# Kernel optimization log

Measured on AMD Instinct MI355X. Metric: run time of the kernel, lower is better.

Reference implementation:

```python
import jax, jax.numpy as jnp
import numpy as np
import math

# Single graph (batch vector identically 0): per-graph topk and global_max_pool
# reduce to static lax.top_k and jnp.max. Pooled edge_index from SAGPooling is
# discarded because KnnEdges rebuilds the graph every layer (no_op=False).
N = 20000      # nodes
HID = 128      # in_channels == hidden_channels
L = 3          # num_layers
RATIO = 0.5    # pool_ratio
K0, KINC = 6, 2  # KnnEdges start_k / k_increment
OUT = 5


def setup_inputs() -> dict:
    key = jax.random.key(0)
    ks = jax.random.split(key, 10)
    s = 0.05  # keep tanh scores unsaturated
    x = jax.random.normal(ks[0], (N, HID), jnp.float32)
    pos = jax.random.uniform(ks[1], (N, 2), jnp.float32) * 100.0
    src = jax.random.randint(ks[2], (N * K0,), 0, N)
    dst = jnp.repeat(jnp.arange(N), K0)
    edge_index = jnp.stack([src, dst]).astype(jnp.int32)  # [2, E], row0=src(j), row1=dst(i)
    return dict(
        x=x, pos=pos, edge_index=edge_index,
        Wrel=jax.random.normal(ks[3], (L, HID, HID), jnp.float32) * s,
        brel=jnp.zeros((L, HID), jnp.float32),
        Wroot=jax.random.normal(ks[4], (L, HID, HID), jnp.float32) * s,
        Wprel=jax.random.normal(ks[5], (L, HID), jnp.float32) * s,
        bprel=jnp.zeros((L,), jnp.float32),
        Wproot=jax.random.normal(ks[6], (L, HID), jnp.float32) * s,
        W1=jax.random.normal(ks[7], (HID * L, HID), jnp.float32) * s,
        b1=jnp.zeros((HID,), jnp.float32),
        W2=jax.random.normal(ks[8], (HID, OUT), jnp.float32) * s,
        b2=jnp.zeros((OUT,), jnp.float32),
    )


def _mean_agg(x, src, dst, n):
    # mean over incoming messages x_j for each target i (PyG aggr='mean'; 0 if isolated)
    ssum = jax.ops.segment_sum(x[src], dst, num_segments=n)
    deg = jax.ops.segment_sum(jnp.ones(src.shape, x.dtype), dst, num_segments=n)
    return ssum / jnp.maximum(deg, 1.0)[:, None]


def reference(x, pos, edge_index, Wrel, brel, Wroot, Wprel, bprel, Wproot, W1, b1, W2, b2):
    src, dst = edge_index[0], edge_index[1]
    n = x.shape[0]
    xs = []
    for i in range(L):
        # GraphConv(aggr='mean'): out_i = W_rel @ mean_j x_j + W_root @ x_i + b
        agg = _mean_agg(x, src, dst, n)
        x = jax.nn.relu(agg @ Wrel[i] + x @ Wroot[i] + brel[i])
        # SAGPooling: score GNN = GraphConv(hid->1, aggr='add'); tanh nonlinearity
        sagg = jax.ops.segment_sum(x[src], dst, num_segments=n)
        score = jnp.tanh(sagg @ Wprel[i] + x @ Wproot[i] + bprel[i])  # [n]
        k_keep = math.ceil(RATIO * n)
        vals, perm = jax.lax.top_k(score, k_keep)
        x = x[perm] * vals[:, None]
        xs.append(jnp.max(x, axis=0))  # global_max_pool (single graph)
        # KnnEdges: pos = pos[perm]; rebuild KNN graph with k = start_k + i*k_increment
        pos = pos[perm]
        n = k_keep
        k = K0 + KINC * i
        d2 = jnp.sum((pos[:, None, :] - pos[None, :, :]) ** 2, axis=-1)  # [n, n]
        d2 = jnp.where(jnp.eye(n, dtype=bool), jnp.inf, d2)  # loop=False
        _, nbr = jax.lax.top_k(-d2, k)  # [n, k] nearest neighbors
        src = nbr.reshape(-1)                 # neighbor j (source)
        dst = jnp.repeat(jnp.arange(n), k)    # query i (target)
    h = jnp.concatenate(xs)  # JumpingKnowledge mode='cat' -> [HID*L]
    h = jax.nn.relu(h @ W1 + b1)  # dropout p=0.5 in eval mode: identity
    return (h @ W2 + b2)[None, :]  # [1, OUT]
```

## Files before the change

### kernel.cpp

```cpp
#include <hip/hip_runtime.h>
#include <hip/hip_bf16.h>
#include <math.h>

#define HID 128
#define PR 20
#define CRPB 32
#define CAND_CAP 8192
#define MAXEQ 8192
#define MAXCELLS 4096

__device__ inline int wave_iscan(int v, int lane) {
#pragma unroll
  for (int off = 1; off < 64; off <<= 1) {
    int o = __shfl_up(v, off, 64);
    if (lane >= off) v += o;
  }
  return v;
}

template <int K>
__global__ __launch_bounds__(256) void k_conv_fused(
    const float* __restrict__ x, const int* __restrict__ src, int n, float invk,
    const float* __restrict__ Wrel, const float* __restrict__ Wroot,
    const float* __restrict__ brel,
    const float* __restrict__ wprel, const float* __restrict__ wproot,
    float* __restrict__ out, float* __restrict__ uo, float* __restrict__ vo) {
  __shared__ float4 sagg4[CRPB][HID / 4];
  __shared__ float4 sx4[CRPB][HID / 4];
  __shared__ int ssrc[CRPB * K];
  int t = threadIdx.x;
  int i0 = blockIdx.x * CRPB;
  const int nK = n * K;
  for (int s = t; s < CRPB * K; s += 256) {
    int gi = i0 * K + s;
    int v = (gi < nK) ? src[gi] : 0;
    ssrc[s] = ((unsigned)v < (unsigned)n) ? v : 0;
  }
  __syncthreads();
  {
    int fq = t & 31, h = t >> 5;
    const float4* x4 = (const float4*)x;
    for (int r = h; r < CRPB; r += 8) {
      int row = i0 + r;
      float4 s = make_float4(0.f, 0.f, 0.f, 0.f);
      float4 xv = make_float4(0.f, 0.f, 0.f, 0.f);
      if (row < n) {
#pragma unroll
        for (int j = 0; j < K; ++j) {
          float4 xx = x4[(size_t)ssrc[r * K + j] * 32 + fq];
          s.x += xx.x; s.y += xx.y; s.z += xx.z; s.w += xx.w;
        }
        xv = x4[(size_t)row * 32 + fq];
      }
      s.x *= invk; s.y *= invk; s.z *= invk; s.w *= invk;
      sagg4[r][fq] = s;
      sx4[r][fq] = xv;
    }
  }
  __syncthreads();
  int q = t & 31, rg = t >> 5;
  const float4* Wrel4  = (const float4*)Wrel;
  const float4* Wroot4 = (const float4*)Wroot;
  float4 bq = ((const float4*)brel)[q];
  float4 acc[4];
#pragma unroll
  for (int rr = 0; rr < 4; ++rr) acc[rr] = bq;
  int rbase = rg * 4;
#pragma unroll 2
  for (int cq = 0; cq < HID / 4; ++cq) {
    float4 w1[4], w2[4];
#pragma unroll
    for (int uu = 0; uu < 4; ++uu) {
      w1[uu] = Wrel4[(cq * 4 + uu) * 32 + q];
      w2[uu] = Wroot4[(cq * 4 + uu) * 32 + q];
    }
#pragma unroll
    for (int rr = 0; rr < 4; ++rr) {
      float4 a  = sagg4[rbase + rr][cq];
      float4 xx = sx4[rbase + rr][cq];
      acc[rr].x += a.x*w1[0].x + a.y*w1[1].x + a.z*w1[2].x + a.w*w1[3].x
                 + xx.x*w2[0].x + xx.y*w2[1].x + xx.z*w2[2].x + xx.w*w2[3].x;
      acc[rr].y += a.x*w1[0].y + a.y*w1[1].y + a.z*w1[2].y + a.w*w1[3].y
                 + xx.x*w2[0].y + xx.y*w2[1].y + xx.z*w2[2].y + xx.w*w2[3].y;
      acc[rr].z += a.x*w1[0].z + a.y*w1[1].z + a.z*w1[2].z + a.w*w1[3].z
                 + xx.x*w2[0].z + xx.y*w2[1].z + xx.z*w2[2].z + xx.w*w2[3].z;
      acc[rr].w += a.x*w1[0].w + a.y*w1[1].w + a.z*w1[2].w + a.w*w1[3].w
                 + xx.x*w2[0].w + xx.y*w2[1].w + xx.z*w2[2].w + xx.w*w2[3].w;
    }
  }
  float4 wplq = ((const float4*)wprel)[q];
  float4 wprq = ((const float4*)wproot)[q];
#pragma unroll
  for (int rr = 0; rr < 4; ++rr) {
    int row = i0 + rbase + rr;
    float4 v = acc[rr];
    v.x = v.x > 0.f ? v.x : 0.f;
    v.y = v.y > 0.f ? v.y : 0.f;
    v.z = v.z > 0.f ? v.z : 0.f;
    v.w = v.w > 0.f ? v.w : 0.f;
    float pu = 0.f, pv = 0.f;
    if (row < n) {
      ((float4*)out)[(size_t)row * 32 + q] = v;
      pu = v.x * wplq.x + v.y * wplq.y + v.z * wplq.z + v.w * wplq.w;
      pv = v.x * wprq.x + v.y * wprq.y + v.z * wprq.z + v.w * wprq.w;
    }
#pragma unroll
    for (int o = 16; o; o >>= 1) {
      pu += __shfl_down(pu, o, 32);
      pv += __shfl_down(pv, o, 32);
    }
    if (q == 0 && row < n) { uo[row] = pu; vo[row] = pv; }
  }
}

template <int K>
__global__ void k_score_lite(const float* __restrict__ u, const float* __restrict__ v,
                             const int* __restrict__ src, const float* __restrict__ bprel,
                             int n, float* __restrict__ score, unsigned* __restrict__ key) {
  int i = blockIdx.x * blockDim.x + threadIdx.x;
  if (i >= n) return;
  float s = v[i] + bprel[0];
#pragma unroll
  for (int j = 0; j < K; ++j) s += u[src[i * K + j]];
  float sc = tanhf(s);
  score[i] = sc;
  unsigned bb = __float_as_uint(sc);
  key[i] = (bb & 0x80000000u) ? ~bb : (bb | 0x80000000u);
}

__global__ __launch_bounds__(128) void k_hist(const unsigned* __restrict__ key, int n4,
                                              unsigned* __restrict__ ghist) {
  __shared__ unsigned lh[1024];
  int t = threadIdx.x;
#pragma unroll
  for (int u = 0; u < 8; ++u) lh[t + u * 128] = 0u;
  __syncthreads();
  int i = blockIdx.x * 128 + t;
  if (i < n4) {
    uint4 kv = ((const uint4*)key)[i];
    atomicAdd(&lh[kv.x >> 22], 1u);
    atomicAdd(&lh[kv.y >> 22], 1u);
    atomicAdd(&lh[kv.z >> 22], 1u);
    atomicAdd(&lh[kv.w >> 22], 1u);
  }
  __syncthreads();
#pragma unroll
  for (int u = 0; u < 8; ++u) {
    unsigned v = lh[t + u * 128];
    if (v) atomicAdd(&ghist[t + u * 128], v);
  }
}

__global__ __launch_bounds__(1024) void k_pick(const unsigned* __restrict__ key, int n, int kk,
                                               const unsigned* __restrict__ ghist,
                                               unsigned* __restrict__ outTG) {
  __shared__ unsigned cand[CAND_CAP];
  __shared__ unsigned hist256[256];
  __shared__ unsigned sh_B, sh_above, sh_cnt, sh_remain, sh_prefix;
  __shared__ int wtA[16], wtB[4];
  int t = threadIdx.x;
  int lane = t & 63, wid = t >> 6;
  unsigned long long lmask = (1ull << lane) - 1ull;
  if (t == 0) sh_cnt = 0u;
  {
    unsigned hv = ghist[t];
    int iv = wave_iscan((int)hv, lane);
    if (lane == 63) wtA[wid] = iv;
    __syncthreads();
    int b = 0, tot = 0;
#pragma unroll
    for (int w2 = 0; w2 < 16; ++w2) { int s = wtA[w2]; if (w2 < wid) b += s; tot += s; }
    unsigned val = (unsigned)(iv + b);
    unsigned above_strict = (unsigned)tot - val;
    unsigned above_incl = above_strict + hv;
    if (above_incl >= (unsigned)kk && above_strict < (unsigned)kk) {
      sh_B = (unsigned)t;
      sh_above = above_strict;
    }
    __syncthreads();
  }
  unsigned B = sh_B, above = sh_above;
  int remain = kk - (int)above;
  for (int i = t; i < n; i += 1024) {
    unsigned kv = key[i];
    bool m = ((kv >> 22) == B);
    unsigned long long mm = __ballot(m);
    if (mm) {
      int leader = (int)(__ffsll((long long)mm) - 1);
      unsigned base = 0;
      if (lane == leader) base = atomicAdd(&sh_cnt, (unsigned)__popcll(mm));
      base = (unsigned)__shfl((int)base, leader, 64);
      if (m) {
        unsigned p = base + (unsigned)__popcll(mm & lmask);
        if (p < CAND_CAP) cand[p] = kv;
      }
    }
  }
  __syncthreads();
  int cnt = (int)sh_cnt; if (cnt > CAND_CAP) cnt = CAND_CAP;
  if (t == 0) { sh_prefix = 0u; sh_remain = (unsigned)remain; }
  __syncthreads();
  for (int pass = 0; pass < 4; ++pass) {
    int shift = 24 - pass * 8;
    unsigned prefix = sh_prefix;
    unsigned rem = sh_remain;
    if (t < 256) hist256[t] = 0u;
    __syncthreads();
    unsigned himask = (pass == 0) ? 0u : (0xFFFFFFFFu << (shift + 8));
    for (int i = t; i < cnt; i += 1024) {
      unsigned kky = cand[i];
      if ((kky & himask) == prefix) atomicAdd(&hist256[(kky >> shift) & 255u], 1u);
    }
    __syncthreads();
    int hv = (t < 256) ? (int)hist256[t] : 0;
    int iv = wave_iscan(hv, lane);
    if (t < 256 && lane == 63) wtB[wid] = iv;
    __syncthreads();
    if (t < 256) {
      int b = 0, tot = 0;
#pragma unroll
      for (int w2 = 0; w2 < 4; ++w2) { int s = wtB[w2]; if (w2 < wid) b += s; tot += s; }
      unsigned val = (unsigned)(iv + b);
      unsigned sstrict = (unsigned)tot - val;
      if (sstrict < rem && sstrict + (unsigned)hv >= rem) {
        sh_prefix = prefix | ((unsigned)t << shift);
        sh_remain = rem - sstrict;
      }
    }
    __syncthreads();
  }
  if (t == 0) {
    outTG[0] = sh_prefix;
    outTG[1] = above + (unsigned)remain - sh_remain;
  }
}

__global__ void k_sel(const unsigned* __restrict__ key, int n,
                      const unsigned* __restrict__ TG,
                      int* __restrict__ perm, int* __restrict__ cntGt,
                      int* __restrict__ eqbuf, int* __restrict__ cntEq) {
  int i = blockIdx.x * blockDim.x + threadIdx.x;
  int lane = threadIdx.x & 63;
  unsigned long long lmask = (1ull << lane) - 1ull;
  unsigned T = TG[0];
  unsigned kv = (i < n) ? key[i] : 0u;
  bool g = (i < n) && (kv > T);
  bool e = (i < n) && (kv == T);
  unsigned long long mg = __ballot(g);
  unsigned long long me = __ballot(e);
  if (mg) {
    int leader = (int)(__ffsll((long long)mg) - 1);
    int base = 0;
    if (lane == leader) base = atomicAdd(cntGt, (int)__popcll(mg));
    base = __shfl(base, leader, 64);
    if (g) perm[base + (int)__popcll(mg & lmask)] = i;
  }
  if (me) {
    int leader = (int)(__ffsll((long long)me) - 1);
    int base = 0;
    if (lane == leader) base = atomicAdd(cntEq, (int)__popcll(me));
    base = __shfl(base, leader, 64);
    if (e) {
      int p = base + (int)__popcll(me & lmask);
      if (p < MAXEQ) eqbuf[p] = i;
    }
  }
}

__global__ void k_sel_eq_fin(const unsigned* __restrict__ TG, const int* __restrict__ eqbuf,
                             const int* __restrict__ cntEq, int* __restrict__ perm, int kk) {
  int lane = threadIdx.x;
  int G = (int)TG[1];
  int need = kk - G;
  int cnt = *cntEq; if (cnt > MAXEQ) cnt = MAXEQ;
  int prev = -1;
  for (int t = 0; t < need; ++t) {
    int mymin = 0x7fffffff;
    for (int u = lane; u < cnt; u += 64) {
      int v = eqbuf[u];
      if (v > prev && v < mymin) mymin = v;
    }
    for (int o = 1; o < 64; o <<= 1) mymin = min(mymin, __shfl_xor(mymin, o, 64));
    if (lane == 0) perm[G + t] = mymin;
    prev = mymin;
  }
}

template <int R>
__global__ __launch_bounds__(256) void k_pool_pmax(
    const float* __restrict__ x, const float* __restrict__ score,
    const int* __restrict__ perm, const float* __restrict__ pos_in,
    float* __restrict__ xout, float* __restrict__ pos_out, int store,
    float* __restrict__ pmax, int* __restrict__ counts, int Gg, float inv_w) {
  __shared__ float sm[2][HID];
  int f = threadIdx.x & 127;
  int half = threadIdx.x >> 7;
  int j0 = blockIdx.x * R;
  float mx = -1e30f;
  for (int r = half; r < R; r += 2) {
    int j = j0 + r;
    int node = perm[j];
    float v = score[node];
    float val = x[(size_t)node * HID + f] * v;
    if (store) {
      xout[(size_t)j * HID + f] = val;
      if (f == 0) {
        float px = pos_in[node * 2], py = pos_in[node * 2 + 1];
        pos_out[j * 2] = px; pos_out[j * 2 + 1] = py;
        int cx = min(Gg - 1, max(0, (int)(px * inv_w)));
        int cy = min(Gg - 1, max(0, (int)(py * inv_w)));
        atomicAdd(&counts[cy * Gg + cx], 1);
      }
    }
    mx = fmaxf(mx, val);
  }
  sm[half][f] = mx;
  __syncthreads();
  if (half == 0) pmax[blockIdx.x * HID + f] = fmaxf(sm[0][f], sm[1][f]);
}

__global__ __launch_bounds__(1024) void k_grid_scan(const int* __restrict__ counts,
                                                    int* __restrict__ starts,
                                                    int* __restrict__ cursor, int cells) {
  __shared__ int wtA[16];
  int t = threadIdx.x;
  int lane = t & 63, wid = t >> 6;
  int c0[4]; int base4 = t * 4; int s = 0;
#pragma unroll
  for (int u = 0; u < 4; ++u) {
    int idx = base4 + u;
    c0[u] = (idx < cells) ? counts[idx] : 0;
    s += c0[u];
  }
  int is = wave_iscan(s, lane);
  if (lane == 63) wtA[wid] = is;
  __syncthreads();
  int b = 0;
#pragma unroll
  for (int w2 = 0; w2 < 16; ++w2) { if (w2 < wid) b += wtA[w2]; }
  int excl = b + is - s;
#pragma unroll
  for (int u = 0; u < 4; ++u) {
    int idx = base4 + u;
    if (idx < cells) { starts[idx] = excl; cursor[idx] = excl; excl += c0[u]; }
  }
}

__global__ void k_grid_scatter(const float2* __restrict__ pos, int m, int Gg, float inv_w,
                               int* __restrict__ cursor, float2* __restrict__ spos,
                               int* __restrict__ sidx) {
  int i = blockIdx.x * blockDim.x + threadIdx.x;
  if (i >= m) return;
  float2 p = pos[i];
  int cx = min(Gg - 1, max(0, (int)(p.x * inv_w)));
  int cy = min(Gg - 1, max(0, (int)(p.y * inv_w)));
  int pp = atomicAdd(&cursor[cy * Gg + cx], 1);
  spos[pp] = p;
  sidx[pp] = i;
}

template <int K>
__global__ __launch_bounds__(256) void k_knn_wave(const float2* __restrict__ spos,
                           const int* __restrict__ sidx,
                           const int* __restrict__ starts, const int* __restrict__ counts,
                           int m, int G, float w, float inv_w, int* __restrict__ src_out) {
  int lane = threadIdx.x & 63;
  int j = blockIdx.x * (blockDim.x >> 6) + (threadIdx.x >> 6);
  if (j >= m) return;
  float2 qp = spos[j];
  int q = sidx[j];
  int cx = min(G - 1, max(0, (int)(qp.x * inv_w)));
  int cy = min(G - 1, max(0, (int)(qp.y * inv_w)));

  float bd[K]; int bi[K];
#pragma unroll
  for (int t = 0; t < K; ++t) { bd[t] = 1e30f; bi[t] = 0; }

  auto scan_span = [&](int s, int e) {
    for (int p = s + lane; p < e; p += 64) {
      if (p == j) continue;
      float2 pp = spos[p];
      float dx = qp.x - pp.x, dy = qp.y - pp.y;
      float d = dx * dx + dy * dy;
      if (d < bd[K - 1]) {
        float dd = d; int ii = sidx[p];
#pragma unroll
        for (int t = 0; t < K; ++t) {
          bool sw = dd < bd[t];
          float od = bd[t]; int oi = bi[t];
          if (sw) { bd[t] = dd; bi[t] = ii; dd = od; ii = oi; }
        }
      }
    }
  };

  {
    int xl = max(0, cx - 1), xh = min(G - 1, cx + 1);
    int y0 = max(0, cy - 1), y1 = min(G - 1, cy + 1);
    int ss[3], ee[3]; int nr = 0;
    for (int y = y0; y <= y1; ++y) {
      int b = y * G;
      ss[nr] = starts[b + xl];
      ee[nr] = starts[b + xh] + counts[b + xh];
      ++nr;
    }
    for (int t = 0; t < nr; ++t) scan_span(ss[t], ee[t]);
  }

  int r = 1;
  unsigned long long mg[K];
  while (true) {
    unsigned long long tmp[K];
#pragma unroll
    for (int t = 0; t < K; ++t)
      tmp[t] = ((unsigned long long)__float_as_uint(bd[t]) << 32) | (unsigned)bi[t];
#pragma unroll
    for (int t = 0; t < K; ++t) {
      unsigned long long mn = tmp[0];
#pragma unroll
      for (int o = 1; o < 64; o <<= 1) {
        unsigned long long ot = __shfl_xor(mn, o, 64);
        if (ot < mn) mn = ot;
      }
      mg[t] = mn;
      if (tmp[0] == mn) {
#pragma unroll
        for (int s2 = 0; s2 < K - 1; ++s2) tmp[s2] = tmp[s2 + 1];
        tmp[K - 1] = ~0ull;
      }
    }
    float kth = __uint_as_float((unsigned)(mg[K - 1] >> 32));
    float bnd = 1e30f;
    if (cx - r > 0)     bnd = fminf(bnd, qp.x - (float)(cx - r) * w);
    if (cx + r < G - 1) bnd = fminf(bnd, (float)(cx + r + 1) * w - qp.x);
    if (cy - r > 0)     bnd = fminf(bnd, qp.y - (float)(cy - r) * w);
    if (cy + r < G - 1) bnd = fminf(bnd, (float)(cy + r + 1) * w - qp.y);
    if (bnd > 1e29f) break;
    float bb = fmaxf(bnd, 0.f) * 0.999f;
    if (kth < bb * bb) break;
    ++r;
    int xl = max(0, cx - r), xh = min(G - 1, cx + r);
    int yt = cy - r, yb = cy + r;
    if (yt >= 0)     { int b = yt * G; scan_span(starts[b + xl], starts[b + xh] + counts[b + xh]); }
    if (yb <= G - 1) { int b = yb * G; scan_span(starts[b + xl], starts[b + xh] + counts[b + xh]); }
    int ylo = max(0, cy - r + 1), yhi = min(G - 1, cy + r - 1);
    for (int y = ylo; y <= yhi; ++y) {
      int b = y * G;
      if (cx - r >= 0)     { int c = b + cx - r; scan_span(starts[c], starts[c] + counts[c]); }
      if (cx + r <= G - 1) { int c = b + cx + r; scan_span(starts[c], starts[c] + counts[c]); }
    }
  }
  if (lane == 0) {
#pragma unroll
    for (int t = 0; t < K; ++t) src_out[q * K + t] = (int)(unsigned)(mg[t] & 0xffffffffu);
  }
}

__global__ __launch_bounds__(1024) void k_final(const float* __restrict__ pmax,
                        int P0, int P1, int P2,
                        const float* __restrict__ W1, const float* __restrict__ b1,
                        const float* __restrict__ W2, const float* __restrict__ b2,
                        float* __restrict__ out) {
  __shared__ float red[8][HID];
  __shared__ float sxs[3 * HID];
  __shared__ float h1[HID];
  int f = threadIdx.x & 127, ch = threadIdx.x >> 7;
  int off0 = 0, off1 = P0, off2 = P0 + P1, off3 = P0 + P1 + P2;
  int lo[3] = {off0, off1, off2};
  int hi[3] = {off1, off2, off3};
  for (int l = 0; l < 3; ++l) {
    float mx = -1e30f;
    for (int p = lo[l] + ch; p < hi[l]; p += 8) mx = fmaxf(mx, pmax[p * HID + f]);
    red[ch][f] = mx;
    __syncthreads();
    if (ch == 0) {
      float m2 = red[0][f];
#pragma unroll
      for (int u = 1; u < 8; ++u) m2 = fmaxf(m2, red[u][f]);
      sxs[l * HID + f] = m2;
    }
    __syncthreads();
  }
  if (threadIdx.x < HID) {
    float acc = b1[f];
    for (int c = 0; c < 3 * HID; ++c) acc += sxs[c] * W1[c * HID + f];
    h1[f] = acc > 0.f ? acc : 0.f;
  }
  __syncthreads();
  if (threadIdx.x < 5) {
    float a = b2[threadIdx.x];
    for (int c = 0; c < HID; ++c) a += h1[c] * W2[c * 5 + threadIdx.x];
    out[threadIdx.x] = a;
  }
}

extern "C" void kernel_launch(void* const* d_in, const int* in_sizes, int n_in,
                              void* d_out, int out_size, void* d_ws, size_t ws_size,
                              hipStream_t stream) {
  const float* x_in   = (const float*)d_in[0];
  const float* pos_in = (const float*)d_in[1];
  const int*   ei     = (const int*)d_in[2];
  const float* Wrel   = (const float*)d_in[3];
  const float* brel   = (const float*)d_in[4];
  const float* Wroot  = (const float*)d_in[5];
  const float* Wprel  = (const float*)d_in[6];
  const float* bprel  = (const float*)d_in[7];
  const float* Wproot = (const float*)d_in[8];
  const float* W1     = (const float*)d_in[9];
  const float* b1     = (const float*)d_in[10];
  const float* W2     = (const float*)d_in[11];
  const float* b2     = (const float*)d_in[12];
  float* out = (float*)d_out;

  const int N0 = in_sizes[0] / HID;
  const int P0 = (N0 / 2) / PR, P1 = (N0 / 4) / PR, P2 = (N0 / 8) / PR;

  char* w = (char*)d_ws;
  float*    xB     = (float*)w;    w += (size_t)N0 * HID * 4;
  float*    xA     = (float*)w;    w += (size_t)(N0 / 2) * HID * 4;
  float*    score  = (float*)w;    w += (size_t)N0 * 4;
  unsigned* key    = (unsigned*)w; w += (size_t)N0 * 4;
  float*    ubuf   = (float*)w;    w += (size_t)N0 * 4;
  float*    vbuf   = (float*)w;    w += (size_t)N0 * 4;
  float*    posA   = (float*)w;    w += (size_t)(N0 / 2) * 2 * 4;
  float*    posB   = (float*)w;    w += (size_t)(N0 / 2) * 2 * 4;
  int*      srcbuf = (int*)w;      w += (size_t)(N0 / 2) * 8 * 4;
  int*      permb  = (int*)w;      w += (size_t)(N0 / 2) * 4;
  float*    pmax   = (float*)w;    w += (size_t)(P0 + P1 + P2) * HID * 4;
  unsigned* ghist  = (unsigned*)w; w += 1024 * 4;
  int*      cnt    = (int*)w;      w += 32;
  int*      counts = (int*)w;      w += MAXCELLS * 4;
  const size_t ZERO_BYTES = 1024 * 4 + 32 + MAXCELLS * 4;
  unsigned* TG     = (unsigned*)w; w += 16;
  int*      eqbuf  = (int*)w;      w += MAXEQ * 4;
  int*      starts = (int*)w;      w += MAXCELLS * 4;
  int*      cursor = (int*)w;      w += MAXCELLS * 4;
  float2*   spos   = (float2*)w;   w += (size_t)(N0 / 2) * 8;
  int*      sidx   = (int*)w;      w += (size_t)(N0 / 2) * 4;
  (void)ws_size; (void)n_in; (void)out_size;

  int n = N0;
  const float* xcur   = x_in;
  const float* poscur = pos_in;
  const int*   srccur = ei;
  int kcur = 6;
  int Poff = 0;

  for (int l = 0; l < 3; ++l) {
    const int kk = n / 2;
    int Gg = (int)ceilf(sqrtf((float)kk / 2.5f));
    if (Gg > 64) Gg = 64;
    if (Gg < 1) Gg = 1;
    int cells = Gg * Gg;
    float cw = 100.f / (float)Gg;
    float inv_w = (float)Gg / 100.f;
    int cblocks = (n + CRPB - 1) / CRPB;

    hipMemsetAsync(ghist, 0, ZERO_BYTES, stream);

    if (kcur == 6) {
      k_conv_fused<6><<<cblocks, 256, 0, stream>>>(xcur, srccur, n, 1.f / 6.f,
          Wrel + l * HID * HID, Wroot + l * HID * HID, brel + l * HID,
          Wprel + l * HID, Wproot + l * HID, xB, ubuf, vbuf);
      k_score_lite<6><<<(n + 255) / 256, 256, 0, stream>>>(ubuf, vbuf, srccur, bprel + l,
                                                           n, score, key);
    } else {
      k_conv_fused<8><<<cblocks, 256, 0, stream>>>(xcur, srccur, n, 1.f / 8.f,
          Wrel + l * HID * HID, Wroot + l * HID * HID, brel + l * HID,
          Wprel + l * HID, Wproot + l * HID, xB, ubuf, vbuf);
      k_score_lite<8><<<(n + 255) / 256, 256, 0, stream>>>(ubuf, vbuf, srccur, bprel + l,
                                                           n, score, key);
    }
    int n4 = n >> 2;
    k_hist<<<(n4 + 127) / 128, 128, 0, stream>>>(key, n4, ghist);
    k_pick<<<1, 1024, 0, stream>>>(key, n, kk, ghist, TG);
    k_sel<<<(n + 255) / 256, 256, 0, stream>>>(key, n, TG, permb, cnt, eqbuf, cnt + 1);
    k_sel_eq_fin<<<1, 64, 0, stream>>>(TG, eqbuf, cnt + 1, permb, kk);

    float* pos_out = (l == 0) ? posA : posB;
    int store = (l < 2) ? 1 : 0;
    k_pool_pmax<PR><<<kk / PR, 256, 0, stream>>>(xB, score, permb, poscur, xA, pos_out,
                                                 store, pmax + (size_t)Poff * HID,
                                                 counts, Gg, inv_w);
    Poff += kk / PR;
    n = kk;
    if (l < 2) {
      k_grid_scan<<<1, 1024, 0, stream>>>(counts, starts, cursor, cells);
      k_grid_scatter<<<(n + 255) / 256, 256, 0, stream>>>((const float2*)pos_out, n, Gg, inv_w,
                                                          cursor, spos, sidx);
      if (l == 0) { k_knn_wave<6><<<(n + 3) / 4, 256, 0, stream>>>(spos, sidx, starts, counts,
                                                                   n, Gg, cw, inv_w, srcbuf); kcur = 6; }
      else        { k_knn_wave<8><<<(n + 3) / 4, 256, 0, stream>>>(spos, sidx, starts, counts,
                                                                   n, Gg, cw, inv_w, srcbuf); kcur = 8; }
    }
    xcur = xA; poscur = pos_out; srccur = srcbuf;
  }
  k_final<<<1, 1024, 0, stream>>>(pmax, P0, P1, P2, W1, b1, W2, b2, out);
}
```

Before: 281.1 us.

## Split single-block top-k pick into grid-wide collect and parallelize final max-pool reduction

The single-block k_pick kernel, which scanned all n keys with 1024 threads, is split into three kernels. k_pickbin finds the threshold bin, a grid-wide k_collect gathers candidate keys into a global buffer with atomics, and k_refine does the radix refinement in one block. The final global max-pool reduction likewise moves from one block into a 24-block k_colmax2 pre-pass, and the first MLP matmul is split across 8 thread groups. This removes serial single-block scans but adds extra kernel launches per layer.

```diff
diff --git a/kernel.cpp b/kernel.cpp
--- a/kernel.cpp
+++ b/kernel.cpp
@@ -151,53 +151,66 @@
   }
 }
 
-__global__ __launch_bounds__(1024) void k_pick(const unsigned* __restrict__ key, int n, int kk,
-                                               const unsigned* __restrict__ ghist,
-                                               unsigned* __restrict__ outTG) {
+__global__ __launch_bounds__(1024) void k_pickbin(const unsigned* __restrict__ ghist, int kk,
+                                                  unsigned* __restrict__ BA) {
+  __shared__ int wtA[16];
+  __shared__ unsigned sh_B, sh_above;
+  int t = threadIdx.x;
+  int lane = t & 63, wid = t >> 6;
+  unsigned hv = ghist[t];
+  int iv = wave_iscan((int)hv, lane);
+  if (lane == 63) wtA[wid] = iv;
+  __syncthreads();
+  int b = 0, tot = 0;
+#pragma unroll
+  for (int w2 = 0; w2 < 16; ++w2) { int s = wtA[w2]; if (w2 < wid) b += s; tot += s; }
+  unsigned val = (unsigned)(iv + b);
+  unsigned above_strict = (unsigned)tot - val;
+  unsigned above_incl = above_strict + hv;
+  if (above_incl >= (unsigned)kk && above_strict < (unsigned)kk) {
+    sh_B = (unsigned)t;
+    sh_above = above_strict;
+  }
+  __syncthreads();
+  if (t == 0) { BA[0] = sh_B; BA[1] = sh_above; }
+}
+
+__global__ void k_collect(const unsigned* __restrict__ key, int n,
+                          const unsigned* __restrict__ BA,
+                          unsigned* __restrict__ candbuf, int* __restrict__ candCnt) {
+  int i = blockIdx.x * blockDim.x + threadIdx.x;
+  int lane = threadIdx.x & 63;
+  unsigned long long lmask = (1ull << lane) - 1ull;
+  unsigned B = BA[0];
+  unsigned kv = (i < n) ? key[i] : 0u;
+  bool m = (i < n) && ((kv >> 22) == B);
+  unsigned long long mm = __ballot(m);
+  if (mm) {
+    int leader = (int)(__ffsll((long long)mm) - 1);
+    int base = 0;
+    if (lane == leader) base = atomicAdd(candCnt, (int)__popcll(mm));
+    base = __shfl(base, leader, 64);
+    if (m) {
+      int p = base + (int)__popcll(mm & lmask);
+      if (p < CAND_CAP) candbuf[p] = kv;
+    }
+  }
+}
+
+__global__ __launch_bounds__(1024) void k_refine(const unsigned* __restrict__ candbuf,
+                                                 const int* __restrict__ candCnt,
+                                                 const unsigned* __restrict__ BA, int kk,
+                                                 unsigned* __restrict__ outTG) {
   __shared__ unsigned cand[CAND_CAP];
   __shared__ unsigned hist256[256];
-  __shared__ unsigned sh_B, sh_above, sh_cnt, sh_remain, sh_prefix;
-  __shared__ int wtA[16], wtB[4];
+  __shared__ unsigned sh_remain, sh_prefix;
+  __shared__ int wtB[4];
   int t = threadIdx.x;
   int lane = t & 63, wid = t >> 6;
-  unsigned long long lmask = (1ull << lane) - 1ull;
-  if (t == 0) sh_cnt = 0u;
-  {
-    unsigned hv = ghist[t];
-    int iv = wave_iscan((int)hv, lane);
-    if (lane == 63) wtA[wid] = iv;
-    __syncthreads();
-    int b = 0, tot = 0;
-#pragma unroll
-    for (int w2 = 0; w2 < 16; ++w2) { int s = wtA[w2]; if (w2 < wid) b += s; tot += s; }
-    unsigned val = (unsigned)(iv + b);
-    unsigned above_strict = (unsigned)tot - val;
-    unsigned above_incl = above_strict + hv;
-    if (above_incl >= (unsigned)kk && above_strict < (unsigned)kk) {
-      sh_B = (unsigned)t;
-      sh_above = above_strict;
-    }
-    __syncthreads();
-  }
-  unsigned B = sh_B, above = sh_above;
+  unsigned B = BA[0], above = BA[1];
   int remain = kk - (int)above;
-  for (int i = t; i < n; i += 1024) {
-    unsigned kv = key[i];
-    bool m = ((kv >> 22) == B);
-    unsigned long long mm = __ballot(m);
-    if (mm) {
-      int leader = (int)(__ffsll((long long)mm) - 1);
-      unsigned base = 0;
-      if (lane == leader) base = atomicAdd(&sh_cnt, (unsigned)__popcll(mm));
-      base = (unsigned)__shfl((int)base, leader, 64);
-      if (m) {
-        unsigned p = base + (unsigned)__popcll(mm & lmask);
-        if (p < CAND_CAP) cand[p] = kv;
-      }
-    }
-  }
-  __syncthreads();
-  int cnt = (int)sh_cnt; if (cnt > CAND_CAP) cnt = CAND_CAP;
+  int cnt = *candCnt; if (cnt > CAND_CAP) cnt = CAND_CAP;
+  for (int i = t; i < cnt; i += 1024) cand[i] = candbuf[i];
   if (t == 0) { sh_prefix = 0u; sh_remain = (unsigned)remain; }
   __syncthreads();
   for (int pass = 0; pass < 4; ++pass) {
@@ -456,35 +469,47 @@
   }
 }
 
-__global__ __launch_bounds__(1024) void k_final(const float* __restrict__ pmax,
-                        int P0, int P1, int P2,
+__global__ __launch_bounds__(256) void k_colmax2(const float* __restrict__ pmax,
+                                                 int P0, int P1, int P2,
+                                                 float* __restrict__ pmax2) {
+  __shared__ float sm[2][HID];
+  int l = blockIdx.x >> 3, c = blockIdx.x & 7;
+  int lo3[3] = {0, P0, P0 + P1};
+  int len3[3] = {P0, P1, P2};
+  int lo = lo3[l], len = len3[l];
+  int f = threadIdx.x & 127, half = threadIdx.x >> 7;
+  float mx = -1e30f;
+  for (int p = c + 8 * half; p < len; p += 16)
+    mx = fmaxf(mx, pmax[(size_t)(lo + p) * HID + f]);
+  sm[half][f] = mx;
+  __syncthreads();
+  if (half == 0) pmax2[(size_t)blockIdx.x * HID + f] = fmaxf(sm[0][f], sm[1][f]);
+}
+
+__global__ __launch_bounds__(1024) void k_final(const float* __restrict__ pmax2,
                         const float* __restrict__ W1, const float* __restrict__ b1,
                         const float* __restrict__ W2, const float* __restrict__ b2,
                         float* __restrict__ out) {
+  __shared__ float sxs[3 * HID];
   __shared__ float red[8][HID];
-  __shared__ float sxs[3 * HID];
   __shared__ float h1[HID];
   int f = threadIdx.x & 127, ch = threadIdx.x >> 7;
-  int off0 = 0, off1 = P0, off2 = P0 + P1, off3 = P0 + P1 + P2;
-  int lo[3] = {off0, off1, off2};
-  int hi[3] = {off1, off2, off3};
-  for (int l = 0; l < 3; ++l) {
-    float mx = -1e30f;
-    for (int p = lo[l] + ch; p < hi[l]; p += 8) mx = fmaxf(mx, pmax[p * HID + f]);
-    red[ch][f] = mx;
-    __syncthreads();
-    if (ch == 0) {
-      float m2 = red[0][f];
-#pragma unroll
-      for (int u = 1; u < 8; ++u) m2 = fmaxf(m2, red[u][f]);
-      sxs[l * HID + f] = m2;
-    }
-    __syncthreads();
-  }
-  if (threadIdx.x < HID) {
-    float acc = b1[f];
-    for (int c = 0; c < 3 * HID; ++c) acc += sxs[c] * W1[c * HID + f];
-    h1[f] = acc > 0.f ? acc : 0.f;
+  if (ch < 3) {
+    float mx = pmax2[(size_t)(ch * 8) * HID + f];
+#pragma unroll
+    for (int u = 1; u < 8; ++u) mx = fmaxf(mx, pmax2[(size_t)(ch * 8 + u) * HID + f]);
+    sxs[ch * HID + f] = mx;
+  }
+  __syncthreads();
+  float acc = 0.f;
+  for (int c = ch * 48; c < (ch + 1) * 48; ++c) acc += sxs[c] * W1[c * HID + f];
+  red[ch][f] = acc;
+  __syncthreads();
+  if (ch == 0) {
+    float a = b1[f];
+#pragma unroll
+    for (int u = 0; u < 8; ++u) a += red[u][f];
+    h1[f] = a > 0.f ? a : 0.f;
   }
   __syncthreads();
   if (threadIdx.x < 5) {
@@ -527,11 +552,14 @@
   int*      srcbuf = (int*)w;      w += (size_t)(N0 / 2) * 8 * 4;
   int*      permb  = (int*)w;      w += (size_t)(N0 / 2) * 4;
   float*    pmax   = (float*)w;    w += (size_t)(P0 + P1 + P2) * HID * 4;
+  float*    pmax2  = (float*)w;    w += (size_t)24 * HID * 4;
   unsigned* ghist  = (unsigned*)w; w += 1024 * 4;
   int*      cnt    = (int*)w;      w += 32;
   int*      counts = (int*)w;      w += MAXCELLS * 4;
   const size_t ZERO_BYTES = 1024 * 4 + 32 + MAXCELLS * 4;
   unsigned* TG     = (unsigned*)w; w += 16;
+  unsigned* BA     = (unsigned*)w; w += 16;
+  unsigned* candbuf= (unsigned*)w; w += CAND_CAP * 4;
   int*      eqbuf  = (int*)w;      w += MAXEQ * 4;
   int*      starts = (int*)w;      w += MAXCELLS * 4;
   int*      cursor = (int*)w;      w += MAXCELLS * 4;
@@ -573,7 +601,9 @@
     }
     int n4 = n >> 2;
     k_hist<<<(n4 + 127) / 128, 128, 0, stream>>>(key, n4, ghist);
-    k_pick<<<1, 1024, 0, stream>>>(key, n, kk, ghist, TG);
+    k_pickbin<<<1, 1024, 0, stream>>>(ghist, kk, BA);
+    k_collect<<<(n + 255) / 256, 256, 0, stream>>>(key, n, BA, candbuf, cnt + 2);
+    k_refine<<<1, 1024, 0, stream>>>(candbuf, cnt + 2, BA, kk, TG);
     k_sel<<<(n + 255) / 256, 256, 0, stream>>>(key, n, TG, permb, cnt, eqbuf, cnt + 1);
     k_sel_eq_fin<<<1, 64, 0, stream>>>(TG, eqbuf, cnt + 1, permb, kk);
 
@@ -595,5 +625,6 @@
     }
     xcur = xA; poscur = pos_out; srccur = srcbuf;
   }
-  k_final<<<1, 1024, 0, stream>>>(pmax, P0, P1, P2, W1, b1, W2, b2, out);
-}
+  k_colmax2<<<24, 256, 0, stream>>>(pmax, P0, P1, P2, pmax2);
+  k_final<<<1, 1024, 0, stream>>>(pmax2, W1, b1, W2, b2, out);
+}
```

Result: faster. 266.4 us (-5.2%).
